# Optimization experiments

Measured on AMD Instinct MI355X. Metric: run time of the kernel, lower is better.

## Reference

```python
import jax, jax.numpy as jnp
import numpy as np

N_NODES = 100000
N_EDGES = 1600000
IN_FEATS = 256
OUT_FEATS = 128


def setup_inputs() -> dict:
    key = jax.random.key(0)
    k1, k2, k3, k4, k5, k6 = jax.random.split(key, 6)
    feat = jax.random.normal(k1, (N_NODES, IN_FEATS), dtype=jnp.float32)
    # xavier_uniform-style scale for the weight
    limit = float(np.sqrt(6.0 / (IN_FEATS + OUT_FEATS)))
    weight = jax.random.uniform(k2, (IN_FEATS, OUT_FEATS), dtype=jnp.float32, minval=-limit, maxval=limit)
    # degree-normalizer scalars per node (positive, like 1/sqrt(deg))
    cj = jax.random.uniform(k3, (N_NODES, 1), dtype=jnp.float32, minval=0.05, maxval=1.0)
    ci = jax.random.uniform(k4, (N_NODES, 1), dtype=jnp.float32, minval=0.05, maxval=1.0)
    src = jax.random.randint(k5, (N_EDGES,), 0, N_NODES, dtype=jnp.int32)
    dst = jax.random.randint(k6, (N_EDGES,), 0, N_NODES, dtype=jnp.int32)
    return {"feat": feat, "weight": weight, "cj": cj, "ci": ci, "src": src, "dst": dst}


def reference(feat, weight, cj, ci, src, dst):
    # dense transform: [N, in] @ [in, out] -> [N, out]
    h = feat @ weight
    # pre-scale by source normalizer (dropout rate 0 -> identity)
    h = h * cj
    # copy_src + sum aggregation: gather messages at src, scatter-sum into dst
    msgs = h[src]  # [E, out]
    agg = jax.ops.segment_sum(msgs, dst, num_segments=N_NODES)  # [N, out]
    # post-scale by destination normalizer
    return agg * ci
```

## Files before the change

kernel.cpp:

```cpp
#include <hip/hip_runtime.h>

#define N_NODES 100000
#define N_EDGES 1600000
#define IN_F 256
#define OUT_F 128
#define E4 (N_EDGES / 4)

#define BUCKETS 256
#define NPB 391
#define CH 8192
#define NCHUNK ((N_EDGES + CH - 1) / CH)
#define CAP 8192

#define GEMM_BLOCKS 1563
#define GB_BLOCKS (GEMM_BLOCKS + BUCKETS)

typedef short bf16x8 __attribute__((ext_vector_type(8)));
typedef float f32x4 __attribute__((ext_vector_type(4)));

__device__ __forceinline__ unsigned int f2bf(float f) {
    unsigned int u = __float_as_uint(f);
    return (u + 0x7FFFu + ((u >> 16) & 1u)) >> 16;
}
__device__ __forceinline__ unsigned int pack2(float a, float b) {
    return f2bf(a) | (f2bf(b) << 16);
}
__device__ __forceinline__ float bf_lo(unsigned int u) { return __uint_as_float(u << 16); }
__device__ __forceinline__ float bf_hi(unsigned int u) { return __uint_as_float(u & 0xFFFF0000u); }

__global__ __launch_bounds__(512) void part_kernel(const float* __restrict__ W,
                                                   unsigned short* __restrict__ Wfrag,
                                                   const int* __restrict__ src,
                                                   const int* __restrict__ dst,
                                                   int* __restrict__ bucket_cursor,
                                                   unsigned int* __restrict__ slab) {
    __shared__ int hist[256];
    __shared__ int hstart[256];
    __shared__ int gbase[256];
    __shared__ unsigned int stage[CH];
    __shared__ unsigned char bstage[CH];

    const int bid = blockIdx.x;
    const int t = threadIdx.x;

    if (bid < 64) {
        int idx = bid * 512 + t;
        int j    = idx & 7;
        int lane = (idx >> 3) & 63;
        int fkt  = idx >> 9;
        int f    = fkt >> 3;
        int kt   = fkt & 7;
        int c    = f * 16 + (lane & 15);
        int k    = kt * 32 + (lane >> 4) * 8 + j;
        Wfrag[idx] = (unsigned short)f2bf(W[k * OUT_F + c]);
    }

    const int e0 = bid * CH;
    int nE = N_EDGES - e0;
    if (nE > CH) nE = CH;
    if (nE < 0) nE = 0;

    if (t < 256) hist[t] = 0;
    __syncthreads();

    int bb[16], rr[16];
    unsigned int pp[16];
    const int4* d4 = reinterpret_cast<const int4*>(dst);
    const int4* s4 = reinterpret_cast<const int4*>(src);
    #pragma unroll
    for (int i = 0; i < 4; ++i) {
        int li = t + i * 512;
        if (li * 4 < nE) {
            int4 d = d4[(e0 >> 2) + li];
            int4 s = s4[(e0 >> 2) + li];
            int b0 = d.x / NPB, b1 = d.y / NPB, b2 = d.z / NPB, b3 = d.w / NPB;
            bb[i*4+0] = b0; pp[i*4+0] = ((unsigned)(d.x - b0 * NPB) << 17) | (unsigned)s.x;
            bb[i*4+1] = b1; pp[i*4+1] = ((unsigned)(d.y - b1 * NPB) << 17) | (unsigned)s.y;
            bb[i*4+2] = b2; pp[i*4+2] = ((unsigned)(d.z - b2 * NPB) << 17) | (unsigned)s.z;
            bb[i*4+3] = b3; pp[i*4+3] = ((unsigned)(d.w - b3 * NPB) << 17) | (unsigned)s.w;
            rr[i*4+0] = atomicAdd(&hist[b0], 1);
            rr[i*4+1] = atomicAdd(&hist[b1], 1);
            rr[i*4+2] = atomicAdd(&hist[b2], 1);
            rr[i*4+3] = atomicAdd(&hist[b3], 1);
        } else {
            bb[i*4+0] = -1; bb[i*4+1] = -1; bb[i*4+2] = -1; bb[i*4+3] = -1;
        }
    }
    __syncthreads();

    int v = 0;
    if (t < 256) { v = hist[t]; hstart[t] = v; }
    __syncthreads();
    #pragma unroll
    for (int off = 1; off < 256; off <<= 1) {
        int u = 0;
        if (t < 256 && t >= off) u = hstart[t - off];
        __syncthreads();
        if (t < 256) hstart[t] += u;
        __syncthreads();
    }
    if (t < 256) {
        int ex = hstart[t] - v;
        if (v > 0) gbase[t] = atomicAdd(&bucket_cursor[t], v);
        hstart[t] = ex;
    }
    __syncthreads();

    #pragma unroll
    for (int i = 0; i < 16; ++i) {
        if (bb[i] >= 0) {
            int pos = hstart[bb[i]] + rr[i];
            stage[pos] = pp[i];
            bstage[pos] = (unsigned char)bb[i];
        }
    }
    __syncthreads();

    for (int idx = t; idx < nE; idx += 512) {
        int b = bstage[idx];
        slab[(size_t)b * CAP + gbase[b] + (idx - hstart[b])] = stage[idx];
    }
}

__global__ __launch_bounds__(256) void gemm_bin_kernel(const float* __restrict__ feat,
                                                       const unsigned short* __restrict__ Wfrag,
                                                       const float* __restrict__ cj,
                                                       unsigned short* __restrict__ h,
                                                       const unsigned int* __restrict__ slab,
                                                       const int* __restrict__ bucket_cursor,
                                                       int* __restrict__ offsets,
                                                       int* __restrict__ bin_src) {
    __shared__ __align__(16) char pool[4 * 16 * 136 * 2];

    const int bid = blockIdx.x;
    const int tid = threadIdx.x;

    if (bid >= GEMM_BLOCKS) {
        int* hist = (int*)pool;
        int* cur  = hist + 392;
        int* sbuf = cur + 392;
        int* gbsz = sbuf + 256;

        const int b = bid - GEMM_BLOCKS;
        const int nlo = b * NPB;
        int nn = N_NODES - nlo;
        if (nn > NPB) nn = NPB;

        int v = bucket_cursor[tid];
        sbuf[tid] = v;
        __syncthreads();
        #pragma unroll
        for (int off = 1; off < 256; off <<= 1) {
            int u = (tid >= off) ? sbuf[tid - off] : 0;
            __syncthreads();
            sbuf[tid] += u;
            __syncthreads();
        }
        if (tid == b) { gbsz[0] = sbuf[tid] - v; gbsz[1] = v; }
        if (b == 0 && tid == 0) offsets[N_NODES] = N_EDGES;
        __syncthreads();
        const int gb = gbsz[0];
        const int sz = gbsz[1];
        const unsigned int* sl = slab + (size_t)b * CAP;

        for (int j = tid; j < 392; j += 256) hist[j] = 0;
        __syncthreads();

        for (int i = tid; i < sz; i += 256) atomicAdd(&hist[sl[i] >> 17], 1);
        __syncthreads();

        int a0 = 0, a1 = 0;
        if (tid < 196) { a0 = hist[2 * tid]; a1 = hist[2 * tid + 1]; }
        int part = a0 + a1;
        sbuf[tid] = part;
        __syncthreads();
        #pragma unroll
        for (int off = 1; off < 256; off <<= 1) {
            int u = (tid >= off) ? sbuf[tid - off] : 0;
            __syncthreads();
            sbuf[tid] += u;
            __syncthreads();
        }
        int ex = sbuf[tid] - part;
        if (tid < 196) {
            int o0 = gb + ex;
            int o1 = o0 + a0;
            if (2 * tid < nn)     { offsets[nlo + 2 * tid]     = o0; cur[2 * tid]     = o0; }
            if (2 * tid + 1 < nn) { offsets[nlo + 2 * tid + 1] = o1; cur[2 * tid + 1] = o1; }
        }
        __syncthreads();

        for (int i = tid; i < sz; i += 256) {
            unsigned int p = sl[i];
            int pos = atomicAdd(&cur[p >> 17], 1);
            bin_src[pos] = (int)(p & 0x1FFFFu);
        }
        return;
    }

    const int wave = tid >> 6;
    const int lane = tid & 63;
    const int r  = lane & 15;
    const int kq = lane >> 4;
    const int rowbase = bid * 64 + wave * 16;
    unsigned short* wout = (unsigned short*)pool + wave * (16 * 136);

    int arow = rowbase + r;
    if (arow >= N_NODES) arow = N_NODES - 1;
    const float4* fr4 = reinterpret_cast<const float4*>(feat + (size_t)arow * IN_F);

    bf16x8 a[8];
    #pragma unroll
    for (int c = 0; c < 2; ++c) {
        float4 fv[8];
        #pragma unroll
        for (int kt = 0; kt < 4; ++kt) {
            fv[2 * kt]     = fr4[(c * 4 + kt) * 8 + kq * 2];
            fv[2 * kt + 1] = fr4[(c * 4 + kt) * 8 + kq * 2 + 1];
        }
        #pragma unroll
        for (int kt = 0; kt < 4; ++kt) {
            uint4 au;
            au.x = pack2(fv[2 * kt].x,     fv[2 * kt].y);
            au.y = pack2(fv[2 * kt].z,     fv[2 * kt].w);
            au.z = pack2(fv[2 * kt + 1].x, fv[2 * kt + 1].y);
            au.w = pack2(fv[2 * kt + 1].z, fv[2 * kt + 1].w);
            a[c * 4 + kt] = *reinterpret_cast<bf16x8*>(&au);
        }
    }

    f32x4 acc[8];
    #pragma unroll
    for (int f = 0; f < 8; ++f) acc[f] = (f32x4){0.f, 0.f, 0.f, 0.f};

    #pragma unroll
    for (int kt = 0; kt < 8; ++kt) {
        #pragma unroll
        for (int f = 0; f < 8; ++f) {
            bf16x8 b = *reinterpret_cast<const bf16x8*>(Wfrag + ((f * 8 + kt) * 64 + lane) * 8);
            acc[f] = __builtin_amdgcn_mfma_f32_16x16x32_bf16(a[kt], b, acc[f], 0, 0, 0);
        }
    }

    int orow[4]; float cjv[4];
    #pragma unroll
    for (int i = 0; i < 4; ++i) {
        orow[i] = rowbase + kq * 4 + i;
        cjv[i] = cj[orow[i] < N_NODES ? orow[i] : 0];
    }

    #pragma unroll
    for (int f = 0; f < 8; ++f) {
        #pragma unroll
        for (int i = 0; i < 4; ++i) {
            wout[(kq * 4 + i) * 136 + f * 16 + r] =
                (unsigned short)f2bf(acc[f][i] * cjv[i]);
        }
    }
    __syncthreads();

    {
        int row = lane >> 2;
        int ch  = lane & 3;
        int grow = rowbase + row;
        if (grow < N_NODES) {
            uint4* hv = reinterpret_cast<uint4*>(h);
            #pragma unroll
            for (int j = 0; j < 4; ++j) {
                uint4 vv = *reinterpret_cast<const uint4*>(
                    (const char*)wout + row * 272 + (ch + 4 * j) * 16);
                hv[(size_t)grow * 16 + ch + 4 * j] = vv;
            }
        }
    }
}

__global__ __launch_bounds__(256) void gather_kernel(const uint4* __restrict__ h4,
                                                     const float* __restrict__ ci,
                                                     const int* __restrict__ offsets,
                                                     const int* __restrict__ bin_src,
                                                     float* __restrict__ out) {
    int node = blockIdx.x * 16 + (threadIdx.x >> 4);
    int lane = threadIdx.x & 15;
    if (node >= N_NODES) return;

    int beg = offsets[node];
    int end = offsets[node + 1];

    float acc[8] = {};
    int i = beg;
    for (; i + 4 <= end; i += 4) {
        int s0 = bin_src[i + 0];
        int s1 = bin_src[i + 1];
        int s2 = bin_src[i + 2];
        int s3 = bin_src[i + 3];
        uint4 v0 = h4[(size_t)s0 * 16 + lane];
        uint4 v1 = h4[(size_t)s1 * 16 + lane];
        uint4 v2 = h4[(size_t)s2 * 16 + lane];
        uint4 v3 = h4[(size_t)s3 * 16 + lane];
        acc[0] += (bf_lo(v0.x) + bf_lo(v1.x)) + (bf_lo(v2.x) + bf_lo(v3.x));
        acc[1] += (bf_hi(v0.x) + bf_hi(v1.x)) + (bf_hi(v2.x) + bf_hi(v3.x));
        acc[2] += (bf_lo(v0.y) + bf_lo(v1.y)) + (bf_lo(v2.y) + bf_lo(v3.y));
        acc[3] += (bf_hi(v0.y) + bf_hi(v1.y)) + (bf_hi(v2.y) + bf_hi(v3.y));
        acc[4] += (bf_lo(v0.z) + bf_lo(v1.z)) + (bf_lo(v2.z) + bf_lo(v3.z));
        acc[5] += (bf_hi(v0.z) + bf_hi(v1.z)) + (bf_hi(v2.z) + bf_hi(v3.z));
        acc[6] += (bf_lo(v0.w) + bf_lo(v1.w)) + (bf_lo(v2.w) + bf_lo(v3.w));
        acc[7] += (bf_hi(v0.w) + bf_hi(v1.w)) + (bf_hi(v2.w) + bf_hi(v3.w));
    }
    for (; i < end; ++i) {
        int s = bin_src[i];
        uint4 v = h4[(size_t)s * 16 + lane];
        acc[0] += bf_lo(v.x); acc[1] += bf_hi(v.x);
        acc[2] += bf_lo(v.y); acc[3] += bf_hi(v.y);
        acc[4] += bf_lo(v.z); acc[5] += bf_hi(v.z);
        acc[6] += bf_lo(v.w); acc[7] += bf_hi(v.w);
    }
    float sc = ci[node];
    float4 o0 = make_float4(acc[0] * sc, acc[1] * sc, acc[2] * sc, acc[3] * sc);
    float4 o1 = make_float4(acc[4] * sc, acc[5] * sc, acc[6] * sc, acc[7] * sc);
    float4* o4 = reinterpret_cast<float4*>(out) + (size_t)node * 32 + lane * 2;
    o4[0] = o0;
    o4[1] = o1;
}

extern "C" void kernel_launch(void* const* d_in, const int* in_sizes, int n_in,
                              void* d_out, int out_size, void* d_ws, size_t ws_size,
                              hipStream_t stream) {
    const float* feat = (const float*)d_in[0];
    const float* W    = (const float*)d_in[1];
    const float* cj   = (const float*)d_in[2];
    const float* ci   = (const float*)d_in[3];
    const int*   src  = (const int*)d_in[4];
    const int*   dst  = (const int*)d_in[5];
    float* out = (float*)d_out;

    const size_t H_BYTES    = (size_t)N_NODES * OUT_F * 2;
    const size_t WT_BYTES   = (size_t)IN_F * OUT_F * 2;
    const size_t OFF_BYTES  = (((size_t)(N_NODES + 1) * 4) + 15) & ~(size_t)15;
    const size_t BC_BYTES   = (((size_t)BUCKETS * 4) + 15) & ~(size_t)15;
    const size_t SLAB_BYTES = (size_t)BUCKETS * CAP * 4;

    char* ws = (char*)d_ws;
    unsigned short* h     = (unsigned short*)ws;  ws += H_BYTES;
    unsigned short* Wfrag = (unsigned short*)ws;  ws += WT_BYTES;
    int* offsets        = (int*)ws;           ws += OFF_BYTES;
    int* bucket_cursor  = (int*)ws;           ws += BC_BYTES;
    unsigned int* slab  = (unsigned int*)ws;  ws += SLAB_BYTES;
    int* bin_src        = (int*)ws;

    hipMemsetAsync(bucket_cursor, 0, (size_t)BUCKETS * 4, stream);

    part_kernel<<<NCHUNK, 512, 0, stream>>>(W, Wfrag, src, dst, bucket_cursor, slab);

    gemm_bin_kernel<<<GB_BLOCKS, 256, 0, stream>>>(feat, Wfrag, cj, h, slab,
                                                   bucket_cursor, offsets, bin_src);

    gather_kernel<<<(N_NODES + 15) / 16, 256, 0, stream>>>((const uint4*)h, ci, offsets, bin_src, out);
}
```

Before: 127.5 us.

## Stage weight fragments through LDS in K-chunks and pipeline feature loads

Reorders the bf16 weight fragment layout to be k-tile major so each 32-wide K pair can be copied contiguously into shared memory. The GEMM now walks K in four chunks. In each chunk the block cooperatively loads the weight slice into LDS while prefetching the next feature slice into registers, then runs MFMAs reading B from LDS instead of global memory. This replaces four waves each reading the weight fragments from global/L2 with one shared copy and fewer live A registers. The cost is extra block barriers per chunk and LDS space shared with the output staging buffer.

```diff
diff --git a/kernel.cpp b/kernel.cpp
--- a/kernel.cpp
+++ b/kernel.cpp
@@ -47,9 +47,9 @@
         int idx = bid * 512 + t;
         int j    = idx & 7;
         int lane = (idx >> 3) & 63;
-        int fkt  = idx >> 9;
-        int f    = fkt >> 3;
-        int kt   = fkt & 7;
+        int ktf  = idx >> 9;
+        int kt   = ktf >> 3;
+        int f    = ktf & 7;
         int c    = f * 16 + (lane & 15);
         int k    = kt * 32 + (lane >> 4) * 8 + j;
         Wfrag[idx] = (unsigned short)f2bf(W[k * OUT_F + c]);
@@ -198,47 +198,70 @@
         return;
     }
 
+    unsigned short* wl = (unsigned short*)pool;
     const int wave = tid >> 6;
     const int lane = tid & 63;
     const int r  = lane & 15;
     const int kq = lane >> 4;
     const int rowbase = bid * 64 + wave * 16;
-    unsigned short* wout = (unsigned short*)pool + wave * (16 * 136);
 
     int arow = rowbase + r;
     if (arow >= N_NODES) arow = N_NODES - 1;
     const float4* fr4 = reinterpret_cast<const float4*>(feat + (size_t)arow * IN_F);
 
-    bf16x8 a[8];
-    #pragma unroll
-    for (int c = 0; c < 2; ++c) {
-        float4 fv[8];
-        #pragma unroll
-        for (int kt = 0; kt < 4; ++kt) {
-            fv[2 * kt]     = fr4[(c * 4 + kt) * 8 + kq * 2];
-            fv[2 * kt + 1] = fr4[(c * 4 + kt) * 8 + kq * 2 + 1];
-        }
-        #pragma unroll
-        for (int kt = 0; kt < 4; ++kt) {
+    f32x4 acc[8];
+    #pragma unroll
+    for (int f = 0; f < 8; ++f) acc[f] = (f32x4){0.f, 0.f, 0.f, 0.f};
+
+    float4 fv[4];
+    fv[0] = fr4[0 * 8 + kq * 2];
+    fv[1] = fr4[0 * 8 + kq * 2 + 1];
+    fv[2] = fr4[1 * 8 + kq * 2];
+    fv[3] = fr4[1 * 8 + kq * 2 + 1];
+
+    const uint4* wsrc = reinterpret_cast<const uint4*>(Wfrag);
+    uint4* wdst = reinterpret_cast<uint4*>(wl);
+
+    for (int c = 0; c < 4; ++c) {
+        if (c > 0) __syncthreads();
+        #pragma unroll
+        for (int i = 0; i < 4; ++i) wdst[tid + i * 256] = wsrc[c * 1024 + tid + i * 256];
+
+        bf16x8 a0, a1;
+        {
             uint4 au;
-            au.x = pack2(fv[2 * kt].x,     fv[2 * kt].y);
-            au.y = pack2(fv[2 * kt].z,     fv[2 * kt].w);
-            au.z = pack2(fv[2 * kt + 1].x, fv[2 * kt + 1].y);
-            au.w = pack2(fv[2 * kt + 1].z, fv[2 * kt + 1].w);
-            a[c * 4 + kt] = *reinterpret_cast<bf16x8*>(&au);
-        }
-    }
-
-    f32x4 acc[8];
-    #pragma unroll
-    for (int f = 0; f < 8; ++f) acc[f] = (f32x4){0.f, 0.f, 0.f, 0.f};
-
-    #pragma unroll
-    for (int kt = 0; kt < 8; ++kt) {
+            au.x = pack2(fv[0].x, fv[0].y);
+            au.y = pack2(fv[0].z, fv[0].w);
+            au.z = pack2(fv[1].x, fv[1].y);
+            au.w = pack2(fv[1].z, fv[1].w);
+            a0 = *reinterpret_cast<bf16x8*>(&au);
+            uint4 bu;
+            bu.x = pack2(fv[2].x, fv[2].y);
+            bu.y = pack2(fv[2].z, fv[2].w);
+            bu.z = pack2(fv[3].x, fv[3].y);
+            bu.w = pack2(fv[3].z, fv[3].w);
+            a1 = *reinterpret_cast<bf16x8*>(&bu);
+        }
+
+        if (c < 3) {
+            int ktb = (c + 1) * 2;
+            fv[0] = fr4[ktb * 8 + kq * 2];
+            fv[1] = fr4[ktb * 8 + kq * 2 + 1];
+            fv[2] = fr4[(ktb + 1) * 8 + kq * 2];
+            fv[3] = fr4[(ktb + 1) * 8 + kq * 2 + 1];
+        }
+
+        __syncthreads();
+
         #pragma unroll
         for (int f = 0; f < 8; ++f) {
-            bf16x8 b = *reinterpret_cast<const bf16x8*>(Wfrag + ((f * 8 + kt) * 64 + lane) * 8);
-            acc[f] = __builtin_amdgcn_mfma_f32_16x16x32_bf16(a[kt], b, acc[f], 0, 0, 0);
+            bf16x8 b = *reinterpret_cast<const bf16x8*>(&wl[((0 * 8 + f) * 64 + lane) * 8]);
+            acc[f] = __builtin_amdgcn_mfma_f32_16x16x32_bf16(a0, b, acc[f], 0, 0, 0);
+        }
+        #pragma unroll
+        for (int f = 0; f < 8; ++f) {
+            bf16x8 b = *reinterpret_cast<const bf16x8*>(&wl[((1 * 8 + f) * 64 + lane) * 8]);
+            acc[f] = __builtin_amdgcn_mfma_f32_16x16x32_bf16(a1, b, acc[f], 0, 0, 0);
         }
     }
 
@@ -249,6 +272,8 @@
         cjv[i] = cj[orow[i] < N_NODES ? orow[i] : 0];
     }
 
+    __syncthreads();
+    unsigned short* wout = (unsigned short*)pool + wave * (16 * 136);
     #pragma unroll
     for (int f = 0; f < 8; ++f) {
         #pragma unroll
```

Measured after the change: 120.3 us. 1.06x faster.

## Stage W fragments in LDS and stream feat loads per k-tile

Applied to the files above, without the earlier changes.

Reorders the precomputed bf16 W fragment layout to be k-tile-major so that each pair of k-tiles forms one contiguous 16KB chunk. The GEMM blocks cooperatively copy that chunk into shared memory, and the per-wave MFMA loop reads B operands from LDS instead of global memory. Feature rows are now loaded one k-tile ahead rather than all up front, which cuts register pressure. A launch-bounds occupancy hint of 8 blocks per CU is added. The trade-off is extra barriers and an LDS round trip per k-tile pair.

```diff
diff --git a/kernel.cpp b/kernel.cpp
--- a/kernel.cpp
+++ b/kernel.cpp
@@ -47,9 +47,9 @@
         int idx = bid * 512 + t;
         int j    = idx & 7;
         int lane = (idx >> 3) & 63;
-        int fkt  = idx >> 9;
-        int f    = fkt >> 3;
-        int kt   = fkt & 7;
+        int ktf  = idx >> 9;
+        int kt   = ktf >> 3;
+        int f    = ktf & 7;
         int c    = f * 16 + (lane & 15);
         int k    = kt * 32 + (lane >> 4) * 8 + j;
         Wfrag[idx] = (unsigned short)f2bf(W[k * OUT_F + c]);
@@ -122,14 +122,14 @@
     }
 }
 
-__global__ __launch_bounds__(256) void gemm_bin_kernel(const float* __restrict__ feat,
-                                                       const unsigned short* __restrict__ Wfrag,
-                                                       const float* __restrict__ cj,
-                                                       unsigned short* __restrict__ h,
-                                                       const unsigned int* __restrict__ slab,
-                                                       const int* __restrict__ bucket_cursor,
-                                                       int* __restrict__ offsets,
-                                                       int* __restrict__ bin_src) {
+__global__ __launch_bounds__(256, 8) void gemm_bin_kernel(const float* __restrict__ feat,
+                                                          const unsigned short* __restrict__ Wfrag,
+                                                          const float* __restrict__ cj,
+                                                          unsigned short* __restrict__ h,
+                                                          const unsigned int* __restrict__ slab,
+                                                          const int* __restrict__ bucket_cursor,
+                                                          int* __restrict__ offsets,
+                                                          int* __restrict__ bin_src) {
     __shared__ __align__(16) char pool[4 * 16 * 136 * 2];
 
     const int bid = blockIdx.x;
@@ -198,47 +198,58 @@
         return;
     }
 
+    unsigned short* wl = (unsigned short*)pool;
     const int wave = tid >> 6;
     const int lane = tid & 63;
     const int r  = lane & 15;
     const int kq = lane >> 4;
     const int rowbase = bid * 64 + wave * 16;
-    unsigned short* wout = (unsigned short*)pool + wave * (16 * 136);
 
     int arow = rowbase + r;
     if (arow >= N_NODES) arow = N_NODES - 1;
     const float4* fr4 = reinterpret_cast<const float4*>(feat + (size_t)arow * IN_F);
 
-    bf16x8 a[8];
-    #pragma unroll
-    for (int c = 0; c < 2; ++c) {
-        float4 fv[8];
-        #pragma unroll
-        for (int kt = 0; kt < 4; ++kt) {
-            fv[2 * kt]     = fr4[(c * 4 + kt) * 8 + kq * 2];
-            fv[2 * kt + 1] = fr4[(c * 4 + kt) * 8 + kq * 2 + 1];
-        }
-        #pragma unroll
-        for (int kt = 0; kt < 4; ++kt) {
+    f32x4 acc[8];
+    #pragma unroll
+    for (int f = 0; f < 8; ++f) acc[f] = (f32x4){0.f, 0.f, 0.f, 0.f};
+
+    float4 fv0 = fr4[kq * 2];
+    float4 fv1 = fr4[kq * 2 + 1];
+
+    const uint4* wsrc = reinterpret_cast<const uint4*>(Wfrag);
+    uint4* wdst = reinterpret_cast<uint4*>(wl);
+
+    #pragma unroll
+    for (int kt = 0; kt < 8; ++kt) {
+        if ((kt & 1) == 0) {
+            if (kt > 0) __syncthreads();
+            #pragma unroll
+            for (int i = 0; i < 4; ++i)
+                wdst[tid + i * 256] = wsrc[(kt >> 1) * 1024 + tid + i * 256];
+        }
+
+        bf16x8 a;
+        {
             uint4 au;
-            au.x = pack2(fv[2 * kt].x,     fv[2 * kt].y);
-            au.y = pack2(fv[2 * kt].z,     fv[2 * kt].w);
-            au.z = pack2(fv[2 * kt + 1].x, fv[2 * kt + 1].y);
-            au.w = pack2(fv[2 * kt + 1].z, fv[2 * kt + 1].w);
-            a[c * 4 + kt] = *reinterpret_cast<bf16x8*>(&au);
-        }
-    }
-
-    f32x4 acc[8];
-    #pragma unroll
-    for (int f = 0; f < 8; ++f) acc[f] = (f32x4){0.f, 0.f, 0.f, 0.f};
-
-    #pragma unroll
-    for (int kt = 0; kt < 8; ++kt) {
+            au.x = pack2(fv0.x, fv0.y);
+            au.y = pack2(fv0.z, fv0.w);
+            au.z = pack2(fv1.x, fv1.y);
+            au.w = pack2(fv1.z, fv1.w);
+            a = *reinterpret_cast<bf16x8*>(&au);
+        }
+
+        if (kt < 7) {
+            fv0 = fr4[(kt + 1) * 8 + kq * 2];
+            fv1 = fr4[(kt + 1) * 8 + kq * 2 + 1];
+        }
+
+        if ((kt & 1) == 0) __syncthreads();
+
+        const int half = (kt & 1) * 8;
         #pragma unroll
         for (int f = 0; f < 8; ++f) {
-            bf16x8 b = *reinterpret_cast<const bf16x8*>(Wfrag + ((f * 8 + kt) * 64 + lane) * 8);
-            acc[f] = __builtin_amdgcn_mfma_f32_16x16x32_bf16(a[kt], b, acc[f], 0, 0, 0);
+            bf16x8 b = *reinterpret_cast<const bf16x8*>(&wl[((half + f) * 64 + lane) * 8]);
+            acc[f] = __builtin_amdgcn_mfma_f32_16x16x32_bf16(a, b, acc[f], 0, 0, 0);
         }
     }
 
@@ -249,6 +260,8 @@
         cjv[i] = cj[orow[i] < N_NODES ? orow[i] : 0];
     }
 
+    __syncthreads();
+    unsigned short* wout = (unsigned short*)pool + wave * (16 * 136);
     #pragma unroll
     for (int f = 0; f < 8; ++f) {
         #pragma unroll
```

New measurement: 118.8 us (median of 2 runs). 6.8% less time.
